# Performance work log

Hardware: AMD Instinct MI355X
Metric: run time of the kernel (lower is better)

The kernel has to match this reference:

```python
import jax, jax.numpy as jnp
import numpy as np

KERNEL = (9, 9, 9)  # box-filter window
KSIZE = KERNEL[0] * KERNEL[1] * KERNEL[2]  # 729
GAMMA = 1.0


def _box_sum(x):
    # x: [B, C, D, H, W] -> channel-sum then 9x9x9 sliding-window sum (SAME pad),
    # exactly matching F.conv3d with an all-ones [1, C, 9,9,9] kernel, pad=4.
    s = jnp.sum(x, axis=1, keepdims=True)  # [B,1,D,H,W]
    return jax.lax.reduce_window(
        s, jnp.asarray(0.0, s.dtype), jax.lax.add,
        window_dimensions=(1, 1) + KERNEL,
        window_strides=(1, 1, 1, 1, 1),
        padding='SAME')


def setup_inputs() -> dict:
    key = jax.random.key(0)
    k1, k2, k3 = jax.random.split(key, 3)
    shape = (2, 1, 160, 160, 160)
    return {
        'input': jax.random.normal(k1, shape, dtype=jnp.float32),
        'target': jax.random.normal(k2, shape, dtype=jnp.float32),
        'flow': jax.random.normal(k3, shape, dtype=jnp.float32),
    }


def reference(input, target, flow):
    # normalize target from (-1, 1) to (0, 1)
    target = (target + 1.0) * 0.5
    w = jax.nn.sigmoid(flow) ** GAMMA  # voxel-wise confidence weight

    T_sum = _box_sum(target)
    I_sum = _box_sum(input)
    TT_sum = _box_sum(target * target)
    II_sum = _box_sum(input * input)
    IT_sum = _box_sum(input * target)

    Ihat = I_sum / KSIZE
    That = T_sum / KSIZE
    cross = IT_sum - Ihat * T_sum - That * I_sum + That * Ihat * KSIZE
    T_var = TT_sum - 2.0 * That * T_sum + That * That * KSIZE
    I_var = II_sum - 2.0 * Ihat * I_sum + Ihat * Ihat * KSIZE

    cc = cross * cross * w / (T_var * I_var + 1e-5)
    return -1.0 * jnp.mean(cc)
```

## Files before the change

### kernel.cpp

```cpp
#include <hip/hip_runtime.h>


constexpr int NB = 2;
constexpr int ND = 160;
constexpr int NH = 160;
constexpr int NW = 160;
constexpr int TH = 16;
constexpr int TW = 16;
constexpr int DCHUNK = 16;
constexpr int NDCH = ND / DCHUNK;
constexpr int NPL = DCHUNK + 8;
constexpr int NIT = NPL + 2;
constexpr int TRS = 20;
constexpr int TFS = 24 * TRS + 4;
constexpr int PRS = 16;
constexpr int PFS = 16 * PRS + 8;
constexpr float INV_K = 1.0f / 729.0f;
constexpr double INV_COUNT = 1.0 / (double(NB) * ND * NH * NW);

__device__ __forceinline__ void issue_load(
    const float* __restrict__ in, const float* __restrict__ tg,
    int b, int dp, int h0, int w0, int idx,
    float4& iv, float4& tv)
{
    iv = make_float4(0.f, 0.f, 0.f, 0.f);
    tv = make_float4(0.f, 0.f, 0.f, 0.f);
    if ((unsigned)idx < 144u && ((unsigned)dp < (unsigned)ND)) {
        int r = idx / 6;
        int q = idx - r * 6;
        int gh = h0 - 4 + r;
        int gw = w0 - 4 + q * 4;
        if (((unsigned)gh < (unsigned)NH) && ((unsigned)gw < (unsigned)NW)) {
            int base = ((b * ND + dp) * NH + gh) * NW + gw;
            iv = *reinterpret_cast<const float4*>(in + base);
            float4 rv = *reinterpret_cast<const float4*>(tg + base);
            tv.x = fmaf(rv.x, 0.5f, 0.5f);
            tv.y = fmaf(rv.y, 0.5f, 0.5f);
            tv.z = fmaf(rv.z, 0.5f, 0.5f);
            tv.w = fmaf(rv.w, 0.5f, 0.5f);
        }
    }
}

#define W9SLIDE(EXPR, FI)                                                  \
    {                                                                      \
        float p0 = (EXPR(0)), p1 = (EXPR(1)), p2 = (EXPR(2)),              \
              p3 = (EXPR(3)), p4 = (EXPR(4)), p5 = (EXPR(5)),              \
              p6 = (EXPR(6)), p7 = (EXPR(7)), p8 = (EXPR(8)),              \
              p9 = (EXPR(9)), p10 = (EXPR(10)), p11 = (EXPR(11));          \
        float s = p0 + p1 + p2 + p3 + p4 + p5 + p6 + p7 + p8;              \
        float4 o;                                                          \
        o.x = s; s += p9 - p0;                                             \
        o.y = s; s += p10 - p1;                                            \
        o.z = s; s += p11 - p2;                                            \
        o.w = s;                                                           \
        *reinterpret_cast<float4*>(outp + (FI) * TFS) = o;                 \
    }

__device__ __forceinline__ void step2q(int tid, const float* __restrict__ inT,
                                       const float* __restrict__ tgT,
                                       float* __restrict__ t5)
{
    const int r = tid >> 2, q = tid & 3;
    const float4* ip = reinterpret_cast<const float4*>(inT + r * 24 + 4 * q);
    const float4* tp = reinterpret_cast<const float4*>(tgT + r * 24 + 4 * q);
    const float4 i0 = ip[0], i1 = ip[1], i2 = ip[2];
    const float4 t0 = tp[0], t1 = tp[1], t2 = tp[2];
    const float ia[12] = {i0.x, i0.y, i0.z, i0.w, i1.x, i1.y, i1.z, i1.w,
                          i2.x, i2.y, i2.z, i2.w};
    const float ta[12] = {t0.x, t0.y, t0.z, t0.w, t1.x, t1.y, t1.z, t1.w,
                          t2.x, t2.y, t2.z, t2.w};
    float* outp = t5 + r * TRS + 4 * q;
    #define E_T(j)  ta[j]
    #define E_I(j)  ia[j]
    #define E_TT(j) (ta[j] * ta[j])
    #define E_II(j) (ia[j] * ia[j])
    #define E_IT(j) (ia[j] * ta[j])
    W9SLIDE(E_T, 0)
    W9SLIDE(E_I, 1)
    W9SLIDE(E_TT, 2)
    W9SLIDE(E_II, 3)
    W9SLIDE(E_IT, 4)
    #undef E_T
    #undef E_I
    #undef E_TT
    #undef E_II
    #undef E_IT
}

__device__ __forceinline__ void hpass(int t, const float* __restrict__ t5,
                                      float* __restrict__ Pb)
{
    const int f = t >> 4;
    const int rem = t & 15;
    const int wq = rem >> 2, hs = rem & 3;
    const float* bp = t5 + f * TFS + hs * 4 * TRS + wq * 4;
    float4 r4[12];
    #pragma unroll
    for (int k = 0; k < 12; ++k)
        r4[k] = *reinterpret_cast<const float4*>(bp + k * TRS);
    float sx = r4[0].x, sy = r4[0].y, sz = r4[0].z, sw = r4[0].w;
    #pragma unroll
    for (int k = 1; k < 9; ++k) {
        sx += r4[k].x; sy += r4[k].y; sz += r4[k].z; sw += r4[k].w;
    }
    float* op = Pb + f * PFS + hs * 4 * PRS + wq * 4;
    *reinterpret_cast<float4*>(op) = make_float4(sx, sy, sz, sw);
    #pragma unroll
    for (int j = 1; j < 4; ++j) {
        sx += r4[8 + j].x - r4[j - 1].x;
        sy += r4[8 + j].y - r4[j - 1].y;
        sz += r4[8 + j].z - r4[j - 1].z;
        sw += r4[8 + j].w - r4[j - 1].w;
        *reinterpret_cast<float4*>(op + j * PRS) = make_float4(sx, sy, sz, sw);
    }
}

__device__ __forceinline__ float cc_value(const float S[5], float flv)
{
    float wgt = 1.0f / (1.0f + __expf(-flv));
    float Ts = S[0], Is = S[1], TTs = S[2], IIs = S[3], ITs = S[4];
    float Ihat = Is * INV_K;
    float That = Ts * INV_K;
    float cross = ITs - Ihat * Ts - That * Is + That * Ihat * 729.0f;
    float T_var = TTs - 2.0f * That * Ts + That * That * 729.0f;
    float I_var = IIs - 2.0f * Ihat * Is + Ihat * Ihat * 729.0f;
    return cross * cross * wgt / (T_var * I_var + 1e-5f);
}

__global__ void __launch_bounds__(256, 4)
cc3d_main(const float* __restrict__ in, const float* __restrict__ tg,
          const float* __restrict__ fl, double* __restrict__ acc_out)
{
    __shared__ __align__(16) float inT[24 * 24];
    __shared__ __align__(16) float tgT[24 * 24];
    __shared__ __align__(16) float tmp5[5 * TFS];
    __shared__ __align__(16) float Pb[5 * PFS];
    __shared__ float red[4];

    const int tid = threadIdx.x;
    const int w0 = blockIdx.x * TW;
    const int h0 = blockIdx.y * TH;
    const int bz = blockIdx.z;
    const int b  = bz / NDCH;
    const int d0 = (bz - b * NDCH) * DCHUNK;
    const int hh = tid >> 4, ww = tid & 15;

    float ring[45];
    #pragma unroll
    for (int i = 0; i < 45; ++i) ring[i] = 0.f;
    float S[5] = {0.f, 0.f, 0.f, 0.f, 0.f};
    float acc = 0.f;
    float flv = 0.f;

    float4 civ, ctv;
    issue_load(in, tg, b, d0 - 4, h0, w0, tid, civ, ctv);

    for (int lb = 0; lb < NIT; lb += 9) {
        #pragma unroll
        for (int li = 0; li < 9; ++li) {
            const int l = lb + li;
            if (l < NIT) {
                if (l < NPL && tid < 144) {
                    reinterpret_cast<float4*>(inT)[tid] = civ;
                    reinterpret_cast<float4*>(tgT)[tid] = ctv;
                }
                if (l >= 2) {
                    const int slot = (li + 7) % 9;
                    #pragma unroll
                    for (int f = 0; f < 5; ++f) {
                        float pn = Pb[f * PFS + hh * PRS + ww];
                        S[f] += pn - ring[f * 9 + slot];
                        ring[f * 9 + slot] = pn;
                    }
                    if (l >= 10) acc += cc_value(S, flv);
                }
                __syncthreads();
                float4 niv = make_float4(0.f, 0.f, 0.f, 0.f), ntv = niv;
                if (l + 1 < NPL)
                    issue_load(in, tg, b, d0 - 3 + l, h0, w0, tid, niv, ntv);
                if (l < NPL && tid < 96)
                    step2q(tid, inT, tgT, tmp5);
                __syncthreads();
                if (l >= 9 && l <= 24) {
                    int dout = d0 + l - 9;
                    flv = fl[((b * ND + dout) * NH + (h0 + hh)) * NW + (w0 + ww)];
                }
                if (l >= 1 && l <= NPL && tid < 80)
                    hpass(tid, tmp5, Pb);
                __syncthreads();
                civ = niv; ctv = ntv;
            }
        }
    }

    #pragma unroll
    for (int off = 32; off > 0; off >>= 1) acc += __shfl_down(acc, off);
    if ((tid & 63) == 0) red[tid >> 6] = acc;
    __syncthreads();
    if (tid == 0) {
        double v = (double)red[0] + (double)red[1] + (double)red[2] + (double)red[3];
        atomicAdd(acc_out, v);
    }
}

__global__ void cc3d_finalize(const double* __restrict__ acc, float* __restrict__ out)
{
    out[0] = (float)(-(acc[0] * INV_COUNT));
}

extern "C" void kernel_launch(void* const* d_in, const int* in_sizes, int n_in,
                              void* d_out, int out_size, void* d_ws, size_t ws_size,
                              hipStream_t stream)
{
    const float* in = (const float*)d_in[0];
    const float* tg = (const float*)d_in[1];
    const float* fl = (const float*)d_in[2];
    float* out = (float*)d_out;
    double* acc = (double*)d_ws;

    hipMemsetAsync(d_ws, 0, sizeof(double), stream);

    dim3 grid(NW / TW, NH / TH, NB * NDCH);
    cc3d_main<<<grid, dim3(256), 0, stream>>>(in, tg, fl, acc);
    cc3d_finalize<<<1, 1, 0, stream>>>(acc, out);
}
```

Before: 184.3 us.

## Stream input planes to LDS via global_load_lds and deepen depth chunks

Replaces the register-staged plane loads with direct global-to-LDS DMA (global_load_lds), moving the target normalization into the per-plane compute step. The LDS halo is pre-filled with zeros and -1, which normalize to zero, and out-of-range depth planes are skipped with validity flags. The pipeline is shortened by one stage, with the horizontal pass run by a separate group of waves. DCHUNK doubles to 32 so fewer halo planes are recomputed per block, at the cost of half as many blocks and less parallelism.

After: 169.1 us. 1.09x faster.

```diff
diff --git a/kernel.cpp b/kernel.cpp
--- a/kernel.cpp
+++ b/kernel.cpp
@@ -7,37 +7,40 @@
 constexpr int NW = 160;
 constexpr int TH = 16;
 constexpr int TW = 16;
-constexpr int DCHUNK = 16;
+constexpr int DCHUNK = 32;
 constexpr int NDCH = ND / DCHUNK;
 constexpr int NPL = DCHUNK + 8;
-constexpr int NIT = NPL + 2;
+constexpr int NIT = NPL + 1;
 constexpr int TRS = 20;
-constexpr int TFS = 24 * TRS + 4;
+constexpr int TFS = 24 * TRS + 8;
 constexpr int PRS = 16;
 constexpr int PFS = 16 * PRS + 8;
 constexpr float INV_K = 1.0f / 729.0f;
 constexpr double INV_COUNT = 1.0 / (double(NB) * ND * NH * NW);
 
-__device__ __forceinline__ void issue_load(
-    const float* __restrict__ in, const float* __restrict__ tg,
-    int b, int dp, int h0, int w0, int idx,
-    float4& iv, float4& tv)
-{
-    iv = make_float4(0.f, 0.f, 0.f, 0.f);
-    tv = make_float4(0.f, 0.f, 0.f, 0.f);
-    if ((unsigned)idx < 144u && ((unsigned)dp < (unsigned)ND)) {
-        int r = idx / 6;
-        int q = idx - r * 6;
+__device__ __forceinline__ void gld_lds16(const float* g, float* l)
+{
+    __builtin_amdgcn_global_load_lds(
+        (const __attribute__((address_space(1))) void*)g,
+        (__attribute__((address_space(3))) void*)l, 16, 0, 0);
+}
+
+__device__ __forceinline__ void dma_plane(const float* __restrict__ in,
+                                          const float* __restrict__ tg,
+                                          float* __restrict__ inT,
+                                          float* __restrict__ tgT,
+                                          int b, int dp, int h0, int w0, int tid)
+{
+    if (tid < 144) {
+        int r = tid / 6;
+        int q = tid - r * 6;
         int gh = h0 - 4 + r;
         int gw = w0 - 4 + q * 4;
+        int wb = (tid >> 6) * 256;
         if (((unsigned)gh < (unsigned)NH) && ((unsigned)gw < (unsigned)NW)) {
             int base = ((b * ND + dp) * NH + gh) * NW + gw;
-            iv = *reinterpret_cast<const float4*>(in + base);
-            float4 rv = *reinterpret_cast<const float4*>(tg + base);
-            tv.x = fmaf(rv.x, 0.5f, 0.5f);
-            tv.y = fmaf(rv.y, 0.5f, 0.5f);
-            tv.z = fmaf(rv.z, 0.5f, 0.5f);
-            tv.w = fmaf(rv.w, 0.5f, 0.5f);
+            gld_lds16(in + base, inT + wb);
+            gld_lds16(tg + base, tgT + wb);
         }
     }
 }
@@ -68,8 +71,10 @@
     const float4 t0 = tp[0], t1 = tp[1], t2 = tp[2];
     const float ia[12] = {i0.x, i0.y, i0.z, i0.w, i1.x, i1.y, i1.z, i1.w,
                           i2.x, i2.y, i2.z, i2.w};
-    const float ta[12] = {t0.x, t0.y, t0.z, t0.w, t1.x, t1.y, t1.z, t1.w,
-                          t2.x, t2.y, t2.z, t2.w};
+    float ta[12] = {t0.x, t0.y, t0.z, t0.w, t1.x, t1.y, t1.z, t1.w,
+                    t2.x, t2.y, t2.z, t2.w};
+    #pragma unroll
+    for (int j = 0; j < 12; ++j) ta[j] = fmaf(ta[j], 0.5f, 0.5f);
     float* outp = t5 + r * TRS + 4 * q;
     #define E_T(j)  ta[j]
     #define E_I(j)  ia[j]
@@ -153,43 +158,39 @@
     float acc = 0.f;
     float flv = 0.f;
 
-    float4 civ, ctv;
-    issue_load(in, tg, b, d0 - 4, h0, w0, tid, civ, ctv);
+    for (int i = tid; i < 576; i += 256) { inT[i] = 0.f; tgT[i] = -1.f; }
+    __syncthreads();
+    if (d0 - 4 >= 0) dma_plane(in, tg, inT, tgT, b, d0 - 4, h0, w0, tid);
 
     for (int lb = 0; lb < NIT; lb += 9) {
         #pragma unroll
         for (int li = 0; li < 9; ++li) {
             const int l = lb + li;
             if (l < NIT) {
-                if (l < NPL && tid < 144) {
-                    reinterpret_cast<float4*>(inT)[tid] = civ;
-                    reinterpret_cast<float4*>(tgT)[tid] = ctv;
-                }
-                if (l >= 2) {
-                    const int slot = (li + 7) % 9;
+                if (l >= 1) {
+                    const bool vz = ((unsigned)(d0 - 5 + l) < (unsigned)ND);
+                    const int slot = (li + 8) % 9;
                     #pragma unroll
                     for (int f = 0; f < 5; ++f) {
-                        float pn = Pb[f * PFS + hh * PRS + ww];
+                        float pn = vz ? Pb[f * PFS + hh * PRS + ww] : 0.f;
                         S[f] += pn - ring[f * 9 + slot];
                         ring[f * 9 + slot] = pn;
                     }
-                    if (l >= 10) acc += cc_value(S, flv);
+                    if (l >= 9) acc += cc_value(S, flv);
                 }
                 __syncthreads();
-                float4 niv = make_float4(0.f, 0.f, 0.f, 0.f), ntv = niv;
-                if (l + 1 < NPL)
-                    issue_load(in, tg, b, d0 - 3 + l, h0, w0, tid, niv, ntv);
-                if (l < NPL && tid < 96)
-                    step2q(tid, inT, tgT, tmp5);
+                const int dpl = d0 - 4 + l;
+                const bool vl = (l < NPL) && ((unsigned)dpl < (unsigned)ND);
+                if (vl && tid < 96) step2q(tid, inT, tgT, tmp5);
                 __syncthreads();
-                if (l >= 9 && l <= 24) {
-                    int dout = d0 + l - 9;
+                if (vl && tid >= 176) hpass(tid - 176, tmp5, Pb);
+                if (l + 1 < NPL && (unsigned)(dpl + 1) < (unsigned)ND)
+                    dma_plane(in, tg, inT, tgT, b, dpl + 1, h0, w0, tid);
+                if (l >= 8 && l < 40) {
+                    int dout = d0 + l - 8;
                     flv = fl[((b * ND + dout) * NH + (h0 + hh)) * NW + (w0 + ww)];
                 }
-                if (l >= 1 && l <= NPL && tid < 80)
-                    hpass(tid, tmp5, Pb);
                 __syncthreads();
-                civ = niv; ctv = ntv;
             }
         }
     }
```
